# Optimization experiments

Hardware: AMD Instinct MI355X
Metric: run time of the kernel (lower is better)

Reference implementation:

```python
import jax, jax.numpy as jnp
import numpy as np
from functools import partial

# --- config (matches init_kwargs cfg) ---
MAX_OBS = 16
MAX_AGENTS = 9
NA = MAX_AGENTS - 1            # 8 neighbor agents
NC = MAX_OBS + 2 * NA          # 32 HOCBF constraint rows
A_MAX = 1.0
W_MAX = 1.0
D_MAX = 10.0
D_OBS = 0.5
D_SAFE = 0.5
DAMPING = 2.0
STIFFNESS = 1.0
W_SLACK = 100.0
B = 65536
N_ITERS = 100   # ADMM iterations for the batched QP solve
RHO = 1.0


def setup_inputs() -> dict:
    key = jax.random.key(0)
    k = jax.random.split(key, 8)
    return {
        "u_nominal": jax.random.normal(k[0], (B, 2), dtype=jnp.float32),
        "v_current": jax.random.uniform(k[1], (B, 1), dtype=jnp.float32),
        "p_obs": jax.random.normal(k[2], (B, MAX_OBS, 2), dtype=jnp.float32),
        "p_agents": jax.random.normal(k[3], (B, NA, 2), dtype=jnp.float32),
        "v_agents_local": jax.random.normal(k[4], (B, NA, 2), dtype=jnp.float32),
        "agent_active": jnp.ones((B, NA), dtype=jnp.float32),
        "obs_active": jnp.ones((B, MAX_OBS), dtype=jnp.float32),
    }


def _build_Gh(v_current, p_obs, p_agents, v_agents_local, agent_active, obs_active):
    """Faithful translation of the G/h constraint construction."""
    # obstacle CBF rows  (v_current is (B,1) and broadcasts against (B,MAX_OBS))
    lx_o, ly_o = p_obs[..., 0], p_obs[..., 1]
    h_obs = lx_o ** 2 + ly_o ** 2 - D_OBS ** 2
    h_dot_obs = -2.0 * lx_o * v_current
    G_obs = jnp.stack([2.0 * lx_o,
                       2.0 * ly_o * v_current,
                       -jnp.ones_like(lx_o)], axis=-1)           # (B, MAX_OBS, 3)
    h_obs_row = (2.0 * v_current ** 2 + DAMPING * h_dot_obs
                 + STIFFNESS * h_obs) * obs_active               # (B, MAX_OBS)

    # inter-agent avoidance rows
    lx_a, ly_a = p_agents[..., 0], p_agents[..., 1]
    v_jx, v_jy = v_agents_local[..., 0], v_agents_local[..., 1]
    h_avoid = lx_a ** 2 + ly_a ** 2 - D_SAFE ** 2
    h_dot_avoid = -2.0 * lx_a * v_current + 2.0 * (lx_a * v_jx + ly_a * v_jy)
    G_av_a = 2.0 * lx_a
    G_av_w = 2.0 * ly_a * v_current - 2.0 * ly_a * v_jx + 2.0 * lx_a * v_jy
    h_ddot_c = (2.0 * v_current ** 2 - 2.0 * v_current * v_jx
                + 2.0 * (-v_current * v_jx + v_jx ** 2 + v_jy ** 2))
    G_avoid = jnp.stack([G_av_a * agent_active,
                         G_av_w * agent_active,
                         jnp.zeros_like(lx_a)], axis=-1)         # (B, NA, 3)
    h_avoid_row = (h_ddot_c + DAMPING * h_dot_avoid + STIFFNESS * h_avoid) * agent_active

    # connectivity rows
    h_conn = D_MAX ** 2 - (lx_a ** 2 + ly_a ** 2)
    h_dot_conn = -h_dot_avoid
    G_conn = jnp.stack([-G_av_a * agent_active,
                        -G_av_w * agent_active,
                        jnp.zeros_like(lx_a)], axis=-1)          # (B, NA, 3)
    h_conn_row = (-h_ddot_c + DAMPING * h_dot_conn + STIFFNESS * h_conn) * agent_active

    G = jnp.concatenate([G_obs, G_avoid, G_conn], axis=1)        # (B, NC, 3)
    h = jnp.concatenate([h_obs_row, h_avoid_row, h_conn_row], axis=1)  # (B, NC)
    return G, h


def _solve_qp(u_ref, G, h):
    """Batched ADMM solve of: min ||u - u_ref||^2 + w_slack*delta^2,
    s.t. [G; box] x <= [h; box_b], x = [u1, u2, delta]."""
    Bn = u_ref.shape[0]
    box_A = jnp.array([[-1., 0., 0.], [1., 0., 0.],
                       [0., -1., 0.], [0., 1., 0.],
                       [0., 0., -1.]], dtype=u_ref.dtype)
    box_b = jnp.array([A_MAX, A_MAX, W_MAX, W_MAX, 0.0], dtype=u_ref.dtype)
    A = jnp.concatenate([G, jnp.broadcast_to(box_A, (Bn, 5, 3))], axis=1)  # (B, m, 3)
    b = jnp.concatenate([h, jnp.broadcast_to(box_b, (Bn, 5))], axis=1)     # (B, m)

    Q = jnp.diag(jnp.array([2.0, 2.0, 2.0 * W_SLACK], dtype=u_ref.dtype))
    q = jnp.concatenate([-2.0 * u_ref, jnp.zeros((Bn, 1), u_ref.dtype)], axis=1)

    M = Q + RHO * jnp.einsum('bki,bkj->bij', A, A)   # (B, 3, 3)
    Minv = jnp.linalg.inv(M)

    def step(carry, _):
        x, z, y = carry
        rhs = -q + jnp.einsum('bkj,bk->bj', A, RHO * z - y)
        x = jnp.einsum('bij,bj->bi', Minv, rhs)
        v = jnp.einsum('bkj,bj->bk', A, x)
        z = jnp.minimum(v + y / RHO, b)
        y = y + RHO * (v - z)
        return (x, z, y), None

    x0 = jnp.zeros((Bn, 3), u_ref.dtype)
    z0 = jnp.minimum(jnp.zeros_like(b), b)
    y0 = jnp.zeros_like(b)
    (x, _, _), _ = jax.lax.scan(step, (x0, z0, y0), None, length=N_ITERS)
    return x


def reference(u_nominal, v_current, p_obs, p_agents, v_agents_local,
              agent_active, obs_active):
    action_scale = jnp.array([A_MAX, W_MAX], dtype=u_nominal.dtype)
    u_ref = u_nominal * action_scale
    G, h = _build_Gh(v_current, p_obs, p_agents, v_agents_local,
                     agent_active, obs_active)
    x = _solve_qp(u_ref, G, h)      # (B, 3) = [u1, u2, delta]
    u_safe = x[:, :2] / action_scale
    return u_safe
```

## Files before the change

kernel.cpp:

```cpp
#include <hip/hip_runtime.h>


constexpr int NITERS = 100;

typedef float v2 __attribute__((ext_vector_type(2)));

static __device__ __forceinline__ v2 pk_fma(v2 a, v2 b, v2 c) {
    v2 d; asm("v_pk_fma_f32 %0, %1, %2, %3" : "=v"(d) : "v"(a), "v"(b), "v"(c)); return d;
}
static __device__ __forceinline__ v2 pk_fma_nc(v2 a, v2 b, v2 c) {
    v2 d; asm("v_pk_fma_f32 %0, %1, %2, %3 neg_lo:[0,0,1] neg_hi:[0,0,1]"
              : "=v"(d) : "v"(a), "v"(b), "v"(c)); return d;
}
static __device__ __forceinline__ v2 pk_add(v2 a, v2 b) {
    v2 d; asm("v_pk_add_f32 %0, %1, %2" : "=v"(d) : "v"(a), "v"(b)); return d;
}
static __device__ __forceinline__ v2 pk_sub(v2 a, v2 b) {
    v2 d; asm("v_pk_add_f32 %0, %1, %2 neg_lo:[0,1] neg_hi:[0,1]"
              : "=v"(d) : "v"(a), "v"(b)); return d;
}
static __device__ __forceinline__ v2 pk_mul(v2 a, v2 b) {
    v2 d; asm("v_pk_mul_f32 %0, %1, %2" : "=v"(d) : "v"(a), "v"(b)); return d;
}
static __device__ __forceinline__ v2 v2abs(v2 a) { return __builtin_elementwise_abs(a); }
static __device__ __forceinline__ v2 vfma_(v2 a, v2 b, v2 c) { return __builtin_elementwise_fma(a, b, c); }
static __device__ __forceinline__ v2 vmin_(v2 a, v2 b)       { return __builtin_elementwise_min(a, b); }

__global__ __launch_bounds__(256, 1)
void cbf_admm_kernel(const float* __restrict__ u_nom,
                     const float* __restrict__ v_cur,
                     const float* __restrict__ p_obs,
                     const float* __restrict__ p_ag,
                     const float* __restrict__ v_ag,
                     const float* __restrict__ ag_act,
                     const float* __restrict__ ob_act,
                     float* __restrict__ out,
                     int B)
{
    const int b = blockIdx.x * blockDim.x + threadIdx.x;
    if (b >= B) return;

    const float v   = v_cur[b];
    const float2 un = *reinterpret_cast<const float2*>(u_nom + 2 * (size_t)b);

    const v2 Z    = {0.f, 0.f};
    const v2 HALF = {0.5f, 0.5f};

    v2 ga2[8], gw2[8], bo2[8];
    v2 sa0 = Z, sa1 = Z, sa2 = Z;
    {
        const float4* po = reinterpret_cast<const float4*>(p_obs + (size_t)b * 32);
        const float2* oa = reinterpret_cast<const float2*>(ob_act + (size_t)b * 16);
        #pragma unroll
        for (int q = 0; q < 8; ++q) {
            const float4 p  = po[q];
            const float2 ac = oa[q];
            const v2 lx = {p.x, p.z};
            const v2 ly = {p.y, p.w};
            const v2 act = {ac.x, ac.y};
            ga2[q] = 2.f * lx;
            gw2[q] = (2.f * v) * ly;
            const v2 h_obs = lx * lx + ly * ly - 0.25f;
            const v2 hdot  = (-2.f * v) * lx;
            const v2 bb = (2.f * v * v + 2.f * hdot + h_obs) * act;
            bo2[q] = bb;
            sa0 = vfma_(ga2[q], bb, sa0);
            sa1 = vfma_(gw2[q], bb, sa1);
            sa2 = sa2 + bb;
        }
    }

    v2 gaa2[4], gwa2[4], ba2[4], bc2[4];
    {
        const float4* pa = reinterpret_cast<const float4*>(p_ag  + (size_t)b * 16);
        const float4* va = reinterpret_cast<const float4*>(v_ag  + (size_t)b * 16);
        const float2* aa = reinterpret_cast<const float2*>(ag_act + (size_t)b * 8);
        #pragma unroll
        for (int q = 0; q < 4; ++q) {
            const float4 p  = pa[q];
            const float4 w4 = va[q];
            const float2 ac = aa[q];
            const v2 lx = {p.x,  p.z},  ly = {p.y,  p.w};
            const v2 vx = {w4.x, w4.z}, vy = {w4.y, w4.w};
            const v2 act = {ac.x, ac.y};
            const v2 d2  = lx * lx + ly * ly;
            const v2 hdot = (-2.f * v) * lx + 2.f * (lx * vx + ly * vy);
            const v2 hddc = (2.f * v * v) + (-4.f * v) * vx + 2.f * (vx * vx + vy * vy);
            gaa2[q] = (2.f * lx) * act;
            gwa2[q] = ((2.f * v) * ly - 2.f * ly * vx + 2.f * lx * vy) * act;
            const v2 ba = (hddc + 2.f * hdot + (d2 - 0.25f)) * act;
            const v2 bc = (-hddc - 2.f * hdot + (100.f - d2)) * act;
            ba2[q] = ba;
            bc2[q] = bc;
            const v2 dba = ba - bc;
            sa0 = vfma_(gaa2[q], dba, sa0);
            sa1 = vfma_(gwa2[q], dba, sa1);
        }
    }
    const float s0 = 2.f * un.x + sa0.x + sa0.y;
    const float s1 = 2.f * un.y + sa1.x + sa1.y;
    const float s2 = -(sa2.x + sa2.y);

    v2 m00 = Z, m01 = Z, m11 = Z, m02 = Z, m12 = Z;
    #pragma unroll
    for (int q = 0; q < 8; ++q) {
        m00 = vfma_(ga2[q], ga2[q], m00);
        m01 = vfma_(ga2[q], gw2[q], m01);
        m11 = vfma_(gw2[q], gw2[q], m11);
        m02 = m02 - ga2[q];
        m12 = m12 - gw2[q];
    }
    #pragma unroll
    for (int q = 0; q < 4; ++q) {
        const v2 g2 = gaa2[q] + gaa2[q];
        m00 = vfma_(g2, gaa2[q], m00);
        m01 = vfma_(g2, gwa2[q], m01);
        m11 = vfma_(gwa2[q] + gwa2[q], gwa2[q], m11);
    }
    const float M00 = m00.x + m00.y + 4.f;
    const float M01 = m01.x + m01.y;
    const float M11 = m11.x + m11.y + 4.f;
    const float M02 = m02.x + m02.y;
    const float M12 = m12.x + m12.y;
    const float M22 = 217.f;
    const float c00 = M11 * M22 - M12 * M12;
    const float c01 = M02 * M12 - M01 * M22;
    const float c02 = M01 * M12 - M02 * M11;
    const float det = M00 * c00 + M01 * c01 + M02 * c02;
    const float id  = 1.f / det;
    const float i00 = c00 * id, i01 = c01 * id, i02 = c02 * id;
    const float i11 = (M00 * M22 - M02 * M02) * id;
    const float i12 = (M01 * M02 - M00 * M12) * id;
    const float i22 = (M00 * M11 - M01 * M01) * id;

    v2 do2[8], da2[4], dc2[4];
    #pragma unroll
    for (int q = 0; q < 8; ++q) do2[q] = vmin_(Z, -bo2[q]);
    #pragma unroll
    for (int q = 0; q < 4; ++q) { da2[q] = vmin_(Z, -ba2[q]); dc2[q] = vmin_(Z, -bc2[q]); }
    float db0 = -1.f, db1 = -1.f, db2 = -1.f, db3 = -1.f, d4 = 0.f;

    float x0 = 0.f, x1 = 0.f, x2 = 0.f;

    #pragma unroll 1
    for (int it = 0; it < NITERS; ++it) {
        v2 A0 = Z, A1 = Z, AT = Z;
        v2 ado[8], ada[4], adc[4];
        #pragma unroll
        for (int q = 0; q < 8; ++q) {
            const v2 ad = v2abs(do2[q]);
            ado[q] = ad;
            A0 = pk_fma(ga2[q], ad, A0);
            A1 = pk_fma(gw2[q], ad, A1);
            AT = pk_add(AT, ad);
        }
        #pragma unroll
        for (int q = 0; q < 4; ++q) {
            const v2 aa = v2abs(da2[q]);  ada[q] = aa;
            const v2 cc = v2abs(dc2[q]);  adc[q] = cc;
            const v2 diff = pk_sub(aa, cc);
            A0 = pk_fma(gaa2[q], diff, A0);
            A1 = pk_fma(gwa2[q], diff, A1);
        }
        const float rb0 = fabsf(db0) - fabsf(db1);
        const float rb1 = fabsf(db2) - fabsf(db3);
        const float r0 = (s0 + rb0) - (A0.x + A0.y);
        const float r1 = (s1 + rb1) - (A1.x + A1.y);
        const float r2 = (s2 + fabsf(d4)) + (AT.x + AT.y);

        x0 = fmaf(i00, r0, fmaf(i01, r1, i02 * r2));
        x1 = fmaf(i01, r0, fmaf(i11, r1, i12 * r2));
        x2 = fmaf(i02, r0, fmaf(i12, r1, i22 * r2));

        const v2 X0 = {x0, x0}, X1 = {x1, x1};
        const float nx2 = -x2;
        const v2 MX2 = {nx2, nx2};
        #pragma unroll
        for (int q = 0; q < 8; ++q) {
            v2 u = pk_fma(HALF, do2[q], pk_sub(MX2, bo2[q]));
            u = pk_fma(HALF, ado[q], u);
            u = pk_fma(gw2[q], X1, u);
            do2[q] = pk_fma(ga2[q], X0, u);
        }
        #pragma unroll
        for (int q = 0; q < 4; ++q) {
            const v2 va_ = pk_fma(gaa2[q], X0, pk_mul(gwa2[q], X1));
            v2 u = pk_fma(HALF, da2[q], pk_sub(va_, ba2[q]));
            da2[q] = pk_fma(HALF, ada[q], u);
            v2 w = pk_fma_nc(HALF, dc2[q], pk_add(va_, bc2[q]));
            dc2[q] = pk_fma(HALF, adc[q], w);
        }
        const float c0m = -x0 - 1.f, c0p = x0 - 1.f;
        const float c1m = -x1 - 1.f, c1p = x1 - 1.f;
        db0 = fmaxf(db0, 0.f) + c0m;
        db1 = fmaxf(db1, 0.f) + c0p;
        db2 = fmaxf(db2, 0.f) + c1m;
        db3 = fmaxf(db3, 0.f) + c1p;
        d4  = fmaxf(d4, 0.f) - x2;
    }

    reinterpret_cast<float2*>(out)[b] = make_float2(x0, x1);
}

extern "C" void kernel_launch(void* const* d_in, const int* in_sizes, int n_in,
                              void* d_out, int out_size, void* d_ws, size_t ws_size,
                              hipStream_t stream) {
    const float* u_nom  = (const float*)d_in[0];
    const float* v_cur  = (const float*)d_in[1];
    const float* p_obs  = (const float*)d_in[2];
    const float* p_ag   = (const float*)d_in[3];
    const float* v_ag   = (const float*)d_in[4];
    const float* ag_act = (const float*)d_in[5];
    const float* ob_act = (const float*)d_in[6];
    float* out = (float*)d_out;

    const int B = in_sizes[1];
    dim3 block(256), grid((B + 255) / 256);
    hipLaunchKernelGGL(cbf_admm_kernel, grid, block, 0, stream,
                       u_nom, v_cur, p_obs, p_ag, v_ag, ag_act, ob_act, out, B);
}
```

Baseline: 43.10 us.

## Split each QP solve across two lanes with DPP lane-swap reductions

Each batch element is now handled by a pair of adjacent lanes. Each lane owns half of the obstacle and agent constraint rows, and the per-iteration partial sums are combined with a DPP lane swap. The launch uses twice as many threads, the occupancy hint moves to 2 blocks per CU, and every other wavefront gets a short s_sleep so the waves are staggered. This aims to raise parallelism and cut per-thread register pressure in the serial 100-iteration loop, at the cost of extra cross-lane ops each iteration and duplicated scalar work (the inverse and the x updates) in both lanes.

```diff
diff --git a/kernel.cpp b/kernel.cpp
--- a/kernel.cpp
+++ b/kernel.cpp
@@ -26,7 +26,11 @@
 static __device__ __forceinline__ v2 vfma_(v2 a, v2 b, v2 c) { return __builtin_elementwise_fma(a, b, c); }
 static __device__ __forceinline__ v2 vmin_(v2 a, v2 b)       { return __builtin_elementwise_min(a, b); }
 
-__global__ __launch_bounds__(256, 1)
+static __device__ __forceinline__ float lane_swap(float x) {
+    return __int_as_float(__builtin_amdgcn_mov_dpp(__float_as_int(x), 0xB1, 0xF, 0xF, true));
+}
+
+__global__ __launch_bounds__(256, 2)
 void cbf_admm_kernel(const float* __restrict__ u_nom,
                      const float* __restrict__ v_cur,
                      const float* __restrict__ p_obs,
@@ -37,22 +41,24 @@
                      float* __restrict__ out,
                      int B)
 {
-    const int b = blockIdx.x * blockDim.x + threadIdx.x;
-    if (b >= B) return;
-
-    const float v   = v_cur[b];
-    const float2 un = *reinterpret_cast<const float2*>(u_nom + 2 * (size_t)b);
+    const int t  = blockIdx.x * blockDim.x + threadIdx.x;
+    const int e  = t >> 1;
+    const int hf = t & 1;
+    if (e >= B) return;
+
+    const float v   = v_cur[e];
+    const float2 un = *reinterpret_cast<const float2*>(u_nom + 2 * (size_t)e);
 
     const v2 Z    = {0.f, 0.f};
     const v2 HALF = {0.5f, 0.5f};
 
-    v2 ga2[8], gw2[8], bo2[8];
+    v2 ga2[4], gw2[4], bo2[4];
     v2 sa0 = Z, sa1 = Z, sa2 = Z;
     {
-        const float4* po = reinterpret_cast<const float4*>(p_obs + (size_t)b * 32);
-        const float2* oa = reinterpret_cast<const float2*>(ob_act + (size_t)b * 16);
-        #pragma unroll
-        for (int q = 0; q < 8; ++q) {
+        const float4* po = reinterpret_cast<const float4*>(p_obs)  + 4 * (size_t)t;
+        const float2* oa = reinterpret_cast<const float2*>(ob_act) + 4 * (size_t)t;
+        #pragma unroll
+        for (int q = 0; q < 4; ++q) {
             const float4 p  = po[q];
             const float2 ac = oa[q];
             const v2 lx = {p.x, p.z};
@@ -70,13 +76,13 @@
         }
     }
 
-    v2 gaa2[4], gwa2[4], ba2[4], bc2[4];
+    v2 gaa2[2], gwa2[2], ba2[2], bc2[2];
     {
-        const float4* pa = reinterpret_cast<const float4*>(p_ag  + (size_t)b * 16);
-        const float4* va = reinterpret_cast<const float4*>(v_ag  + (size_t)b * 16);
-        const float2* aa = reinterpret_cast<const float2*>(ag_act + (size_t)b * 8);
-        #pragma unroll
-        for (int q = 0; q < 4; ++q) {
+        const float4* pa = reinterpret_cast<const float4*>(p_ag)   + 2 * (size_t)t;
+        const float4* va = reinterpret_cast<const float4*>(v_ag)   + 2 * (size_t)t;
+        const float2* aa = reinterpret_cast<const float2*>(ag_act) + 2 * (size_t)t;
+        #pragma unroll
+        for (int q = 0; q < 2; ++q) {
             const float4 p  = pa[q];
             const float4 w4 = va[q];
             const float2 ac = aa[q];
@@ -97,13 +103,10 @@
             sa1 = vfma_(gwa2[q], dba, sa1);
         }
     }
-    const float s0 = 2.f * un.x + sa0.x + sa0.y;
-    const float s1 = 2.f * un.y + sa1.x + sa1.y;
-    const float s2 = -(sa2.x + sa2.y);
 
     v2 m00 = Z, m01 = Z, m11 = Z, m02 = Z, m12 = Z;
     #pragma unroll
-    for (int q = 0; q < 8; ++q) {
+    for (int q = 0; q < 4; ++q) {
         m00 = vfma_(ga2[q], ga2[q], m00);
         m01 = vfma_(ga2[q], gw2[q], m01);
         m11 = vfma_(gw2[q], gw2[q], m11);
@@ -111,17 +114,24 @@
         m12 = m12 - gw2[q];
     }
     #pragma unroll
-    for (int q = 0; q < 4; ++q) {
+    for (int q = 0; q < 2; ++q) {
         const v2 g2 = gaa2[q] + gaa2[q];
         m00 = vfma_(g2, gaa2[q], m00);
         m01 = vfma_(g2, gwa2[q], m01);
         m11 = vfma_(gwa2[q] + gwa2[q], gwa2[q], m11);
     }
-    const float M00 = m00.x + m00.y + 4.f;
-    const float M01 = m01.x + m01.y;
-    const float M11 = m11.x + m11.y + 4.f;
-    const float M02 = m02.x + m02.y;
-    const float M12 = m12.x + m12.y;
+
+    const float s0p = sa0.x + sa0.y, s1p = sa1.x + sa1.y, s2p = sa2.x + sa2.y;
+    const float s0 = fmaf(2.f, un.x, s0p + lane_swap(s0p));
+    const float s1 = fmaf(2.f, un.y, s1p + lane_swap(s1p));
+    const float s2 = -(s2p + lane_swap(s2p));
+    const float M00p = m00.x + m00.y, M01p = m01.x + m01.y, M11p = m11.x + m11.y;
+    const float M02p = m02.x + m02.y, M12p = m12.x + m12.y;
+    const float M00 = M00p + lane_swap(M00p) + 4.f;
+    const float M01 = M01p + lane_swap(M01p);
+    const float M11 = M11p + lane_swap(M11p) + 4.f;
+    const float M02 = M02p + lane_swap(M02p);
+    const float M12 = M12p + lane_swap(M12p);
     const float M22 = 217.f;
     const float c00 = M11 * M22 - M12 * M12;
     const float c01 = M02 * M12 - M01 * M22;
@@ -133,21 +143,23 @@
     const float i12 = (M01 * M02 - M00 * M12) * id;
     const float i22 = (M00 * M11 - M01 * M01) * id;
 
-    v2 do2[8], da2[4], dc2[4];
-    #pragma unroll
-    for (int q = 0; q < 8; ++q) do2[q] = vmin_(Z, -bo2[q]);
-    #pragma unroll
-    for (int q = 0; q < 4; ++q) { da2[q] = vmin_(Z, -ba2[q]); dc2[q] = vmin_(Z, -bc2[q]); }
+    v2 do2[4], da2[2], dc2[2];
+    #pragma unroll
+    for (int q = 0; q < 4; ++q) do2[q] = vmin_(Z, -bo2[q]);
+    #pragma unroll
+    for (int q = 0; q < 2; ++q) { da2[q] = vmin_(Z, -ba2[q]); dc2[q] = vmin_(Z, -bc2[q]); }
     float db0 = -1.f, db1 = -1.f, db2 = -1.f, db3 = -1.f, d4 = 0.f;
 
     float x0 = 0.f, x1 = 0.f, x2 = 0.f;
+
+    if ((threadIdx.x >> 6) & 1) __builtin_amdgcn_s_sleep(8);
 
     #pragma unroll 1
     for (int it = 0; it < NITERS; ++it) {
         v2 A0 = Z, A1 = Z, AT = Z;
-        v2 ado[8], ada[4], adc[4];
-        #pragma unroll
-        for (int q = 0; q < 8; ++q) {
+        v2 ado[4], ada[2], adc[2];
+        #pragma unroll
+        for (int q = 0; q < 4; ++q) {
             const v2 ad = v2abs(do2[q]);
             ado[q] = ad;
             A0 = pk_fma(ga2[q], ad, A0);
@@ -155,18 +167,22 @@
             AT = pk_add(AT, ad);
         }
         #pragma unroll
-        for (int q = 0; q < 4; ++q) {
-            const v2 aa = v2abs(da2[q]);  ada[q] = aa;
-            const v2 cc = v2abs(dc2[q]);  adc[q] = cc;
-            const v2 diff = pk_sub(aa, cc);
+        for (int q = 0; q < 2; ++q) {
+            const v2 aa_ = v2abs(da2[q]);  ada[q] = aa_;
+            const v2 cc_ = v2abs(dc2[q]);  adc[q] = cc_;
+            const v2 diff = pk_sub(aa_, cc_);
             A0 = pk_fma(gaa2[q], diff, A0);
             A1 = pk_fma(gwa2[q], diff, A1);
         }
         const float rb0 = fabsf(db0) - fabsf(db1);
         const float rb1 = fabsf(db2) - fabsf(db3);
-        const float r0 = (s0 + rb0) - (A0.x + A0.y);
-        const float r1 = (s1 + rb1) - (A1.x + A1.y);
-        const float r2 = (s2 + fabsf(d4)) + (AT.x + AT.y);
+        const float R0p = fmaf(-0.5f, rb0, A0.x + A0.y);
+        const float R1p = fmaf(-0.5f, rb1, A1.x + A1.y);
+        const float R2p = fmaf( 0.5f, fabsf(d4), AT.x + AT.y);
+
+        const float r0 = s0 - (R0p + lane_swap(R0p));
+        const float r1 = s1 - (R1p + lane_swap(R1p));
+        const float r2 = s2 + (R2p + lane_swap(R2p));
 
         x0 = fmaf(i00, r0, fmaf(i01, r1, i02 * r2));
         x1 = fmaf(i01, r0, fmaf(i11, r1, i12 * r2));
@@ -176,30 +192,31 @@
         const float nx2 = -x2;
         const v2 MX2 = {nx2, nx2};
         #pragma unroll
-        for (int q = 0; q < 8; ++q) {
+        for (int q = 0; q < 4; ++q) {
             v2 u = pk_fma(HALF, do2[q], pk_sub(MX2, bo2[q]));
             u = pk_fma(HALF, ado[q], u);
             u = pk_fma(gw2[q], X1, u);
             do2[q] = pk_fma(ga2[q], X0, u);
         }
         #pragma unroll
-        for (int q = 0; q < 4; ++q) {
+        for (int q = 0; q < 2; ++q) {
             const v2 va_ = pk_fma(gaa2[q], X0, pk_mul(gwa2[q], X1));
             v2 u = pk_fma(HALF, da2[q], pk_sub(va_, ba2[q]));
             da2[q] = pk_fma(HALF, ada[q], u);
             v2 w = pk_fma_nc(HALF, dc2[q], pk_add(va_, bc2[q]));
             dc2[q] = pk_fma(HALF, adc[q], w);
         }
-        const float c0m = -x0 - 1.f, c0p = x0 - 1.f;
-        const float c1m = -x1 - 1.f, c1p = x1 - 1.f;
-        db0 = fmaxf(db0, 0.f) + c0m;
-        db1 = fmaxf(db1, 0.f) + c0p;
-        db2 = fmaxf(db2, 0.f) + c1m;
-        db3 = fmaxf(db3, 0.f) + c1p;
+        const float e0 = x0 + 1.f, e1 = x0 - 1.f;
+        const float e2 = x1 + 1.f, e3 = x1 - 1.f;
+        db0 = fmaxf(db0, 0.f) - e0;
+        db1 = fmaxf(db1, 0.f) + e1;
+        db2 = fmaxf(db2, 0.f) - e2;
+        db3 = fmaxf(db3, 0.f) + e3;
         d4  = fmaxf(d4, 0.f) - x2;
     }
 
-    reinterpret_cast<float2*>(out)[b] = make_float2(x0, x1);
+    if (hf == 0)
+        reinterpret_cast<float2*>(out)[e] = make_float2(x0, x1);
 }
 
 extern "C" void kernel_launch(void* const* d_in, const int* in_sizes, int n_in,
@@ -215,7 +232,8 @@
     float* out = (float*)d_out;
 
     const int B = in_sizes[1];
-    dim3 block(256), grid((B + 255) / 256);
+    const int threads = 2 * B;
+    dim3 block(256), grid((threads + 255) / 256);
     hipLaunchKernelGGL(cbf_admm_kernel, grid, block, 0, stream,
                        u_nom, v_cur, p_obs, p_ag, v_ag, ag_act, ob_act, out, B);
 }
```

New measurement: 48.62 us. +12.8%, slower.
